# Kernel tuning notes

Measured on AMD Instinct MI355X. Metric: run time of the kernel, lower is better.

Reference implementation:

```python
import jax, jax.numpy as jnp
import numpy as np

HIDDEN = 1024
HEADS = 16
HEAD_DIM = HIDDEN // HEADS
B, S = 2, 2048


def setup_inputs() -> dict:
    key = jax.random.key(0)
    ks = jax.random.split(key, 11)
    std = 1.0 / np.sqrt(HIDDEN)
    return {
        "query": jax.random.normal(ks[0], (B, S, HIDDEN), dtype=jnp.float32),
        "key": jax.random.normal(ks[1], (B, S, HIDDEN), dtype=jnp.float32),
        "value": jax.random.normal(ks[2], (B, S, HIDDEN), dtype=jnp.float32),
        "Wq": jax.random.uniform(ks[3], (HIDDEN, HIDDEN), jnp.float32, -std, std),
        "bq": jax.random.uniform(ks[4], (HIDDEN,), jnp.float32, -std, std),
        "Wk": jax.random.uniform(ks[5], (HIDDEN, HIDDEN), jnp.float32, -std, std),
        "bk": jax.random.uniform(ks[6], (HIDDEN,), jnp.float32, -std, std),
        "Wv": jax.random.uniform(ks[7], (HIDDEN, HIDDEN), jnp.float32, -std, std),
        "bv": jax.random.uniform(ks[8], (HIDDEN,), jnp.float32, -std, std),
        "Wo": jax.random.uniform(ks[9], (HIDDEN, HIDDEN), jnp.float32, -std, std),
        "bo": jax.random.uniform(ks[10], (HIDDEN,), jnp.float32, -std, std),
    }


def reference(query, key, value, Wq, bq, Wk, bk, Wv, bv, Wo, bo):
    b = query.shape[0]
    scale = jnp.sqrt(jnp.float32(HEAD_DIM))
    # linear projections (torch Linear: x @ W.T + b), split into heads -> [b, h, s, d]
    def proj(x, W, bias):
        y = x @ W.T + bias
        return y.reshape(b, -1, HEADS, HEAD_DIM).transpose(0, 2, 1, 3)
    Q = proj(query, Wq, bq)
    K = proj(key, Wk, bk)
    V = proj(value, Wv, bv)
    scores = jnp.einsum("bhqd,bhkd->bhqk", Q, K) / scale
    attn = jax.nn.softmax(scores, axis=-1)
    ctx = jnp.einsum("bhqk,bhkd->bhqd", attn, V)
    ctx = ctx.transpose(0, 2, 1, 3).reshape(b, -1, HIDDEN)
    return ctx @ Wo.T + bo
```

## Files before the change

kernel.cpp:

```cpp
#include <hip/hip_runtime.h>

typedef __attribute__((ext_vector_type(8))) short short8;
typedef __attribute__((ext_vector_type(2))) float float2_t;
typedef __attribute__((ext_vector_type(4))) float float4_t;
typedef __attribute__((ext_vector_type(16))) float f32x16;
typedef __attribute__((ext_vector_type(4))) unsigned int uint4_t;
typedef __attribute__((ext_vector_type(2))) unsigned int uint2_t;
typedef unsigned short u16;

#define HIDDEN 1024
#define HDIM   64
#define SS     2048
#define TOK    4096
#define QSCALE 0.1803368801111137f

__device__ __forceinline__ unsigned int fbits(float f) {
  unsigned int x; __builtin_memcpy(&x, &f, 4); return x;
}
__device__ __forceinline__ u16 f2bf(float f) {
  return (u16)((fbits(f) + 0x8000u) >> 16);
}
__device__ __forceinline__ unsigned int pk2bf(float a, float b) {
  return __builtin_amdgcn_perm(fbits(b) + 0x8000u, fbits(a) + 0x8000u, 0x07060302);
}
__device__ __forceinline__ unsigned int pk2bf_t(float a, float b) {
  return __builtin_amdgcn_perm(fbits(b), fbits(a), 0x07060302);
}

__device__ __forceinline__ void gl_lds16(const u16* g, u16* l) {
  __builtin_amdgcn_global_load_lds(
      (const __attribute__((address_space(1))) unsigned int*)g,
      (__attribute__((address_space(3))) unsigned int*)l, 16, 0, 0);
}

__global__ __launch_bounds__(256) void convert_all(
    const float* __restrict__ w0, const float* __restrict__ w1,
    const float* __restrict__ w2, const float* __restrict__ w3,
    const float* __restrict__ x0, const float* __restrict__ x1,
    const float* __restrict__ x2, u16* __restrict__ Wall, u16* __restrict__ Xall) {
  int y = blockIdx.y;
  const float* src; u16* dst;
  if (y < 4) {
    if (blockIdx.x >= 512) return;
    src = y == 0 ? w0 : y == 1 ? w1 : y == 2 ? w2 : w3;
    dst = Wall + ((size_t)y << 20);
  } else {
    src = y == 4 ? x0 : y == 5 ? x1 : x2;
    dst = Xall + ((size_t)(y - 4) << 22);
  }
  int g = (blockIdx.x * 256 + threadIdx.x) * 8;
  float4_t a = *(const float4_t*)(src + g);
  float4_t b = *(const float4_t*)(src + g + 4);
  uint4_t o;
  o.x = pk2bf(a[0], a[1]); o.y = pk2bf(a[2], a[3]);
  o.z = pk2bf(b[0], b[1]); o.w = pk2bf(b[2], b[3]);
  *(uint4_t*)(dst + g) = o;
}

template<int MTILES, bool AXF32, bool OUTF32>
__device__ __forceinline__ void gemm_dbuf(
    const void* __restrict__ X, const u16* __restrict__ Wb,
    const float* __restrict__ bias, void* __restrict__ Y, int mode, float oscale,
    u16* sA, u16* sB, int row0, int col0) {
  const int tid  = threadIdx.x;
  const int wv   = tid >> 6, lane = tid & 63, quad = lane >> 4, ln = lane & 15;
  const int wm   = (wv >> 1) * (MTILES * 16), wn = (wv & 1) * 64;
  constexpr int ASZ = MTILES * 32 * 64;
  constexpr int BSZ = 128 * 64;

  float4_t acc[MTILES][4];
#pragma unroll
  for (int i = 0; i < MTILES; i++)
#pragma unroll
    for (int j = 0; j < 4; j++) acc[i][j] = (float4_t)0.0f;

  auto stageB = [&](int buf, int kt) {
    const int k0 = kt * 64;
#pragma unroll
    for (int i = 0; i < 4; i++) {
      int idx = i * 256 + tid, r = idx >> 3, c = idx & 7;
      int gc = c ^ (r & 7);
      gl_lds16(Wb + (size_t)(col0 + r) * HIDDEN + k0 + gc * 8, sB + buf * BSZ + idx * 8);
    }
  };
  auto stageA_bf16 = [&](int buf, int kt) {
    const int k0 = kt * 64;
#pragma unroll
    for (int i = 0; i < MTILES; i++) {
      int idx = i * 256 + tid, r = idx >> 3, c = idx & 7;
      int gc = c ^ (r & 7);
      gl_lds16((const u16*)X + (size_t)(row0 + r) * HIDDEN + k0 + gc * 8,
               sA + buf * ASZ + idx * 8);
    }
  };
  auto loadA_f32 = [&](int kt, float4_t (&ax)[MTILES][2]) {
    const int k0 = kt * 64;
#pragma unroll
    for (int i = 0; i < MTILES; i++) {
      int idx = i * 256 + tid, r = idx >> 3, c = idx & 7;
      const float* p = (const float*)X + (size_t)(row0 + r) * HIDDEN + k0 + c * 8;
      ax[i][0] = *(const float4_t*)p;
      ax[i][1] = *(const float4_t*)(p + 4);
    }
  };
  auto writeA_f32 = [&](int buf, float4_t (&ax)[MTILES][2]) {
#pragma unroll
    for (int i = 0; i < MTILES; i++) {
      int idx = i * 256 + tid, r = idx >> 3, c = idx & 7;
      int pos = c ^ (r & 7);
      union { unsigned int u[4]; short8 s; } x;
      x.u[0] = pk2bf(ax[i][0][0], ax[i][0][1]); x.u[1] = pk2bf(ax[i][0][2], ax[i][0][3]);
      x.u[2] = pk2bf(ax[i][1][0], ax[i][1][1]); x.u[3] = pk2bf(ax[i][1][2], ax[i][1][3]);
      *(short8*)(sA + buf * ASZ + r * 64 + pos * 8) = x.s;
    }
  };

  if (AXF32) {
    float4_t ax0[MTILES][2];
    loadA_f32(0, ax0);
    stageB(0, 0);
    writeA_f32(0, ax0);
  } else {
    stageB(0, 0);
    stageA_bf16(0, 0);
  }
  __syncthreads();

#pragma unroll 2
  for (int kt = 0; kt < 16; ++kt) {
    const int cur = kt & 1;
    float4_t axn[MTILES][2];
    if (AXF32) { if (kt < 15) loadA_f32(kt + 1, axn); }
    if (kt < 15) {
      stageB(cur ^ 1, kt + 1);
      if (!AXF32) stageA_bf16(cur ^ 1, kt + 1);
    }
    const u16* A_ = sA + cur * ASZ;
    const u16* B_ = sB + cur * BSZ;

    short8 af[MTILES][2], bfr[4][2];
#pragma unroll
    for (int mt = 0; mt < MTILES; mt++)
#pragma unroll
      for (int kk = 0; kk < 2; kk++) {
        int r = wm + mt * 16 + ln;
        int ch = kk * 4 + quad;
        af[mt][kk] = *(const short8*)(A_ + r * 64 + (ch ^ (r & 7)) * 8);
      }
#pragma unroll
    for (int nt = 0; nt < 4; nt++)
#pragma unroll
      for (int kk = 0; kk < 2; kk++) {
        int r = wn + nt * 16 + ln;
        int ch = kk * 4 + quad;
        bfr[nt][kk] = *(const short8*)(B_ + r * 64 + (ch ^ (r & 7)) * 8);
      }
#pragma unroll
    for (int kk = 0; kk < 2; kk++)
#pragma unroll
      for (int mt = 0; mt < MTILES; mt++)
#pragma unroll
        for (int nt = 0; nt < 4; nt++)
          acc[mt][nt] = __builtin_amdgcn_mfma_f32_16x16x32_bf16(af[mt][kk], bfr[nt][kk], acc[mt][nt], 0, 0, 0);

    if (AXF32) { if (kt < 15) writeA_f32(cur ^ 1, axn); }
    __syncthreads();
  }

  float bcol[4];
#pragma unroll
  for (int nt = 0; nt < 4; nt++) bcol[nt] = bias[col0 + wn + nt * 16 + ln];
#pragma unroll
  for (int mt = 0; mt < MTILES; mt++)
#pragma unroll
    for (int nt = 0; nt < 4; nt++) {
      int n = col0 + wn + nt * 16 + ln;
#pragma unroll
      for (int r = 0; r < 4; r++) {
        int m = row0 + wm + mt * 16 + quad * 4 + r;
        float v = (acc[mt][nt][r] + bcol[nt]) * oscale;
        if (mode == 0) {
          if (OUTF32) ((float*)Y)[(size_t)m * HIDDEN + n] = v;
          else        ((u16*)Y)[(size_t)m * HIDDEN + n] = f2bf(v);
        } else {
          ((u16*)Y)[((size_t)(m >> 11) * HIDDEN + n) * SS + (m & 2047)] = f2bf(v);
        }
      }
    }
}

__global__ __launch_bounds__(256) void qkv_gemm_bf16(
    const u16* __restrict__ Xall, const u16* __restrict__ Wall,
    const float* __restrict__ bq, const float* __restrict__ bk, const float* __restrict__ bv,
    u16* __restrict__ Qp, u16* __restrict__ Kp, u16* __restrict__ Vt) {
  __shared__ u16 sA[2 * 128 * 64];
  __shared__ u16 sB[2 * 128 * 64];
  int z = blockIdx.z;
  int fid = blockIdx.x, g = fid & 7, j = fid >> 3;
  int xb = j & 7, yb = g + 8 * (j >> 3);
  const u16* X = Xall + ((size_t)z << 22);
  const u16* W = Wall + ((size_t)z << 20);
  const float* Bp = z == 0 ? bq : z == 1 ? bk : bv;
  u16* Y = z == 0 ? Qp : z == 1 ? Kp : Vt;
  int mode = (z == 2) ? 1 : 0;
  float sc = (z == 0) ? QSCALE : 1.0f;
  gemm_dbuf<4, false, false>(X, W, Bp, Y, mode, sc, sA, sB, yb * 128, xb * 128);
}

__global__ __launch_bounds__(256) void qkv_gemm_f32(
    const float* __restrict__ xq, const float* __restrict__ xk, const float* __restrict__ xv,
    const u16* __restrict__ Wall,
    const float* __restrict__ bq, const float* __restrict__ bk, const float* __restrict__ bv,
    u16* __restrict__ Qp, u16* __restrict__ Kp, u16* __restrict__ Vt) {
  __shared__ u16 sA[2 * 128 * 64];
  __shared__ u16 sB[2 * 128 * 64];
  int z = blockIdx.z;
  int fid = blockIdx.x, g = fid & 7, j = fid >> 3;
  int xb = j & 7, yb = g + 8 * (j >> 3);
  const float* X = z == 0 ? xq : z == 1 ? xk : xv;
  const u16* W = Wall + ((size_t)z << 20);
  const float* Bp = z == 0 ? bq : z == 1 ? bk : bv;
  u16* Y = z == 0 ? Qp : z == 1 ? Kp : Vt;
  int mode = (z == 2) ? 1 : 0;
  float sc = (z == 0) ? QSCALE : 1.0f;
  gemm_dbuf<4, true, false>(X, W, Bp, Y, mode, sc, sA, sB, yb * 128, xb * 128);
}

__global__ __launch_bounds__(256) void out_gemm(
    const u16* __restrict__ X, const u16* __restrict__ Wob,
    const float* __restrict__ bias, float* __restrict__ Y) {
  __shared__ u16 sA[2 * 64 * 64];
  __shared__ u16 sB[2 * 128 * 64];
  int fid = blockIdx.x, g = fid & 7, j = fid >> 3;
  int xb = j & 7, yb = g + 8 * (j >> 3);
  gemm_dbuf<2, false, true>(X, Wob, bias, Y, 0, 1.0f, sA, sB, yb * 64, xb * 128);
}

__global__ __launch_bounds__(256, 2) void attn(
    const u16* __restrict__ Qp, const u16* __restrict__ Kp,
    const u16* __restrict__ Vt, u16* __restrict__ Ctx) {
  __shared__ u16 sK[2][128 * 64];
  __shared__ u16 sV[2][64 * 128];
  const int tid  = threadIdx.x;
  const int wv   = tid >> 6, lane = tid & 63;
  const int l5   = lane >> 5, ln = lane & 31;
  const int f = blockIdx.x;
  const int qt = f >> 5, g = f & 31, h = g >> 1, b = g & 1;
  const int row0w = qt * 128 + wv * 32;

  short8 qf[4];
#pragma unroll
  for (int kk = 0; kk < 4; ++kk)
    qf[kk] = *(const short8*)(Qp + (size_t)(b * SS + row0w + ln) * HIDDEN
                              + h * HDIM + kk * 16 + l5 * 8);

  f32x16 oacc[2];
  oacc[0] = (f32x16)0.0f; oacc[1] = (f32x16)0.0f;
  float dsum = 0.f;

  auto stage = [&](int buf, int kt) {
#pragma unroll
    for (int p = 0; p < 4; ++p) {
      int off = p * 256 + tid;
      { int r = off >> 3, c = off & 7;  int gc = c ^ (r & 7);
        gl_lds16(Kp + (size_t)(b * SS + kt * 128 + r) * HIDDEN + h * HDIM + gc * 8,
                 &sK[buf][0] + off * 8); }
      { int r = off >> 4, c = off & 15; int gc = c ^ (r & 15);
        gl_lds16(Vt + ((size_t)b * HIDDEN + h * HDIM + r) * SS + kt * 128 + gc * 8,
                 &sV[buf][0] + off * 8); }
    }
  };

  stage(0, 0);
  __syncthreads();

#pragma unroll 2
  for (int kt = 0; kt < 16; ++kt) {
    const int cur = kt & 1;
    if (kt < 15) stage(cur ^ 1, kt + 1);
    const u16* K_ = &sK[cur][0];
    const u16* V_ = &sV[cur][0];

    f32x16 st[4];
    __builtin_amdgcn_s_setprio(1);
#pragma unroll
    for (int kgg = 0; kgg < 4; ++kgg) {
      st[kgg] = (f32x16)0.0f;
#pragma unroll
      for (int kk = 0; kk < 4; ++kk) {
        int r = kgg * 32 + ln;
        int ch = kk * 2 + l5;
        short8 kf = *(const short8*)(K_ + r * 64 + ((ch ^ (r & 7))) * 8);
        st[kgg] = __builtin_amdgcn_mfma_f32_32x32x16_bf16(kf, qf[kk], st[kgg], 0, 0, 0);
      }
    }
    __builtin_amdgcn_s_setprio(0);

#pragma unroll
    for (int kgg = 0; kgg < 4; ++kgg) {
      union PF { unsigned int u[4]; short8 s; };
      PF pfr[2];
      {
        float p[16];
#pragma unroll
        for (int r = 0; r < 16; ++r)
          p[r] = __builtin_amdgcn_exp2f(fminf(st[kgg][r], 80.f));
        float2_t t0 = (float2_t){p[0], p[1]}   + (float2_t){p[2], p[3]};
        float2_t t1 = (float2_t){p[4], p[5]}   + (float2_t){p[6], p[7]};
        float2_t t2 = (float2_t){p[8], p[9]}   + (float2_t){p[10], p[11]};
        float2_t t3 = (float2_t){p[12], p[13]} + (float2_t){p[14], p[15]};
        float2_t t4 = (t0 + t1) + (t2 + t3);
        dsum += t4.x + t4.y;
        unsigned int pk[8];
#pragma unroll
        for (int i = 0; i < 8; ++i) pk[i] = pk2bf_t(p[2 * i], p[2 * i + 1]);
        uint2_t r02 = __builtin_amdgcn_permlane32_swap(pk[0], pk[2], false, false);
        uint2_t r13 = __builtin_amdgcn_permlane32_swap(pk[1], pk[3], false, false);
        uint2_t r46 = __builtin_amdgcn_permlane32_swap(pk[4], pk[6], false, false);
        uint2_t r57 = __builtin_amdgcn_permlane32_swap(pk[5], pk[7], false, false);
        pfr[0].u[0] = r02.x; pfr[0].u[1] = r13.x;
        pfr[0].u[2] = r02.y; pfr[0].u[3] = r13.y;
        pfr[1].u[0] = r46.x; pfr[1].u[1] = r57.x;
        pfr[1].u[2] = r46.y; pfr[1].u[3] = r57.y;
      }

      __builtin_amdgcn_s_setprio(1);
#pragma unroll
      for (int ks = 0; ks < 2; ++ks) {
        int ch = (kgg * 2 + ks) * 2 + l5;
#pragma unroll
        for (int dg = 0; dg < 2; ++dg) {
          int r = dg * 32 + ln;
          short8 vf = *(const short8*)(V_ + r * 128 + ((ch ^ (r & 15))) * 8);
          oacc[dg] = __builtin_amdgcn_mfma_f32_32x32x16_bf16(vf, pfr[ks].s, oacc[dg], 0, 0, 0);
        }
      }
      __builtin_amdgcn_s_setprio(0);
    }
    __syncthreads();
  }

  float s = dsum + __shfl_xor(dsum, 32, 64);
  float inv = 1.0f / s;

  u16* ep = ((u16*)sK) + wv * 2048;
  {
    int row = ln;
#pragma unroll
    for (int dg = 0; dg < 2; ++dg)
#pragma unroll
      for (int i = 0; i < 4; ++i) {
        uint2_t w;
        w.x = pk2bf(oacc[dg][4 * i] * inv,     oacc[dg][4 * i + 1] * inv);
        w.y = pk2bf(oacc[dg][4 * i + 2] * inv, oacc[dg][4 * i + 3] * inv);
        int c = dg * 4 + i;
        *(uint2_t*)(ep + row * 64 + ((c ^ (row & 7))) * 8 + l5 * 4) = w;
      }
  }
#pragma unroll
  for (int ps = 0; ps < 4; ++ps) {
    int r = ps * 8 + (lane >> 3);
    int c = lane & 7;
    short8 o8 = *(const short8*)(ep + r * 64 + ((c ^ (r & 7))) * 8);
    *(short8*)(Ctx + (size_t)(b * SS + row0w + r) * HIDDEN + h * HDIM + c * 8) = o8;
  }
}

extern "C" void kernel_launch(void* const* d_in, const int* in_sizes, int n_in,
                              void* d_out, int out_size, void* d_ws, size_t ws_size,
                              hipStream_t stream) {
  const float* q  = (const float*)d_in[0];
  const float* k  = (const float*)d_in[1];
  const float* v  = (const float*)d_in[2];
  const float* Wq = (const float*)d_in[3];
  const float* bq = (const float*)d_in[4];
  const float* Wk = (const float*)d_in[5];
  const float* bk = (const float*)d_in[6];
  const float* Wv = (const float*)d_in[7];
  const float* bv = (const float*)d_in[8];
  const float* Wo = (const float*)d_in[9];
  const float* bo = (const float*)d_in[10];

  u16* Qp   = (u16*)d_ws;
  u16* Kp   = Qp + (size_t)TOK * HIDDEN;
  u16* Vt   = Kp + (size_t)TOK * HIDDEN;
  u16* Wall = Vt + (size_t)TOK * HIDDEN;
  u16* Xall = Wall + (4u << 20);
  u16* Cx   = Qp;
  bool useX = ws_size >= (size_t)56 * 1024 * 1024;

  dim3 blk(256);
  if (useX) {
    hipLaunchKernelGGL(convert_all, dim3(2048, 7), blk, 0, stream,
                       Wq, Wk, Wv, Wo, q, k, v, Wall, Xall);
    hipLaunchKernelGGL(qkv_gemm_bf16, dim3(256, 1, 3), blk, 0, stream,
                       Xall, Wall, bq, bk, bv, Qp, Kp, Vt);
  } else {
    hipLaunchKernelGGL(convert_all, dim3(512, 4), blk, 0, stream,
                       Wq, Wk, Wv, Wo, q, k, v, Wall, Wall);
    hipLaunchKernelGGL(qkv_gemm_f32, dim3(256, 1, 3), blk, 0, stream,
                       q, k, v, Wall, bq, bk, bv, Qp, Kp, Vt);
  }
  hipLaunchKernelGGL(attn, dim3(512), blk, 0, stream, Qp, Kp, Vt, Cx);
  hipLaunchKernelGGL(out_gemm, dim3(512), blk, 0, stream,
                     Cx, Wall + (3u << 20), bo, (float*)d_out);
}
```

Before: 220.2 us.

## Pipeline bf16 GEMM loads two tiles ahead with explicit vmcnt waits

Splits the GEMM helper into a bf16-input path and an fp32-input path. The bf16 path (QKV bf16 GEMM and output GEMM) now issues direct-to-LDS loads two K-tiles ahead into the double buffer. It waits on them with partial s_waitcnt vmcnt counts and raw barriers instead of a full __syncthreads per iteration. This is meant to keep global loads in flight across the MFMA work, at the cost of a hand-counted vmcnt that must match the exact number of loads issued.

```diff
diff --git a/kernel.cpp b/kernel.cpp
--- a/kernel.cpp
+++ b/kernel.cpp
@@ -57,9 +57,9 @@
   *(uint4_t*)(dst + g) = o;
 }
 
-template<int MTILES, bool AXF32, bool OUTF32>
-__device__ __forceinline__ void gemm_dbuf(
-    const void* __restrict__ X, const u16* __restrict__ Wb,
+template<int MTILES, bool OUTF32>
+__device__ __forceinline__ void gemm_ctd(
+    const u16* __restrict__ X, const u16* __restrict__ Wb,
     const float* __restrict__ bias, void* __restrict__ Y, int mode, float oscale,
     u16* sA, u16* sB, int row0, int col0) {
   const int tid  = threadIdx.x;
@@ -67,6 +67,7 @@
   const int wm   = (wv >> 1) * (MTILES * 16), wn = (wv & 1) * 64;
   constexpr int ASZ = MTILES * 32 * 64;
   constexpr int BSZ = 128 * 64;
+  constexpr int NLOADS = MTILES + 4;
 
   float4_t acc[MTILES][4];
 #pragma unroll
@@ -74,7 +75,7 @@
 #pragma unroll
     for (int j = 0; j < 4; j++) acc[i][j] = (float4_t)0.0f;
 
-  auto stageB = [&](int buf, int kt) {
+  auto stage = [&](int buf, int kt) {
     const int k0 = kt * 64;
 #pragma unroll
     for (int i = 0; i < 4; i++) {
@@ -82,15 +83,105 @@
       int gc = c ^ (r & 7);
       gl_lds16(Wb + (size_t)(col0 + r) * HIDDEN + k0 + gc * 8, sB + buf * BSZ + idx * 8);
     }
-  };
-  auto stageA_bf16 = [&](int buf, int kt) {
-    const int k0 = kt * 64;
 #pragma unroll
     for (int i = 0; i < MTILES; i++) {
       int idx = i * 256 + tid, r = idx >> 3, c = idx & 7;
       int gc = c ^ (r & 7);
-      gl_lds16((const u16*)X + (size_t)(row0 + r) * HIDDEN + k0 + gc * 8,
-               sA + buf * ASZ + idx * 8);
+      gl_lds16(X + (size_t)(row0 + r) * HIDDEN + k0 + gc * 8, sA + buf * ASZ + idx * 8);
+    }
+  };
+
+  stage(0, 0);
+  stage(1, 1);
+  asm volatile("s_waitcnt vmcnt(%0)" :: "n"(NLOADS) : "memory");
+  __builtin_amdgcn_s_barrier();
+
+#pragma unroll 2
+  for (int kt = 0; kt < 16; ++kt) {
+    const int cur = kt & 1;
+    const u16* A_ = sA + cur * ASZ;
+    const u16* B_ = sB + cur * BSZ;
+
+    short8 af[MTILES][2], bfr[4][2];
+#pragma unroll
+    for (int mt = 0; mt < MTILES; mt++)
+#pragma unroll
+      for (int kk = 0; kk < 2; kk++) {
+        int r = wm + mt * 16 + ln;
+        int ch = kk * 4 + quad;
+        af[mt][kk] = *(const short8*)(A_ + r * 64 + (ch ^ (r & 7)) * 8);
+      }
+#pragma unroll
+    for (int nt = 0; nt < 4; nt++)
+#pragma unroll
+      for (int kk = 0; kk < 2; kk++) {
+        int r = wn + nt * 16 + ln;
+        int ch = kk * 4 + quad;
+        bfr[nt][kk] = *(const short8*)(B_ + r * 64 + (ch ^ (r & 7)) * 8);
+      }
+#pragma unroll
+    for (int kk = 0; kk < 2; kk++)
+#pragma unroll
+      for (int mt = 0; mt < MTILES; mt++)
+#pragma unroll
+        for (int nt = 0; nt < 4; nt++)
+          acc[mt][nt] = __builtin_amdgcn_mfma_f32_16x16x32_bf16(af[mt][kk], bfr[nt][kk], acc[mt][nt], 0, 0, 0);
+
+    __builtin_amdgcn_s_barrier();
+    if (kt < 14) stage(cur, kt + 2);
+    if (kt < 15) {
+      if (kt < 14) asm volatile("s_waitcnt vmcnt(%0)" :: "n"(NLOADS) : "memory");
+      else         asm volatile("s_waitcnt vmcnt(0)" ::: "memory");
+      __builtin_amdgcn_s_barrier();
+    }
+  }
+
+  float bcol[4];
+#pragma unroll
+  for (int nt = 0; nt < 4; nt++) bcol[nt] = bias[col0 + wn + nt * 16 + ln];
+#pragma unroll
+  for (int mt = 0; mt < MTILES; mt++)
+#pragma unroll
+    for (int nt = 0; nt < 4; nt++) {
+      int n = col0 + wn + nt * 16 + ln;
+#pragma unroll
+      for (int r = 0; r < 4; r++) {
+        int m = row0 + wm + mt * 16 + quad * 4 + r;
+        float v = (acc[mt][nt][r] + bcol[nt]) * oscale;
+        if (mode == 0) {
+          if (OUTF32) ((float*)Y)[(size_t)m * HIDDEN + n] = v;
+          else        ((u16*)Y)[(size_t)m * HIDDEN + n] = f2bf(v);
+        } else {
+          ((u16*)Y)[((size_t)(m >> 11) * HIDDEN + n) * SS + (m & 2047)] = f2bf(v);
+        }
+      }
+    }
+}
+
+template<int MTILES, bool OUTF32>
+__device__ __forceinline__ void gemm_dbuf_f32(
+    const float* __restrict__ X, const u16* __restrict__ Wb,
+    const float* __restrict__ bias, void* __restrict__ Y, int mode, float oscale,
+    u16* sA, u16* sB, int row0, int col0) {
+  const int tid  = threadIdx.x;
+  const int wv   = tid >> 6, lane = tid & 63, quad = lane >> 4, ln = lane & 15;
+  const int wm   = (wv >> 1) * (MTILES * 16), wn = (wv & 1) * 64;
+  constexpr int ASZ = MTILES * 32 * 64;
+  constexpr int BSZ = 128 * 64;
+
+  float4_t acc[MTILES][4];
+#pragma unroll
+  for (int i = 0; i < MTILES; i++)
+#pragma unroll
+    for (int j = 0; j < 4; j++) acc[i][j] = (float4_t)0.0f;
+
+  auto stageB = [&](int buf, int kt) {
+    const int k0 = kt * 64;
+#pragma unroll
+    for (int i = 0; i < 4; i++) {
+      int idx = i * 256 + tid, r = idx >> 3, c = idx & 7;
+      int gc = c ^ (r & 7);
+      gl_lds16(Wb + (size_t)(col0 + r) * HIDDEN + k0 + gc * 8, sB + buf * BSZ + idx * 8);
     }
   };
   auto loadA_f32 = [&](int kt, float4_t (&ax)[MTILES][2]) {
@@ -98,7 +189,7 @@
 #pragma unroll
     for (int i = 0; i < MTILES; i++) {
       int idx = i * 256 + tid, r = idx >> 3, c = idx & 7;
-      const float* p = (const float*)X + (size_t)(row0 + r) * HIDDEN + k0 + c * 8;
+      const float* p = X + (size_t)(row0 + r) * HIDDEN + k0 + c * 8;
       ax[i][0] = *(const float4_t*)p;
       ax[i][1] = *(const float4_t*)(p + 4);
     }
@@ -115,14 +206,11 @@
     }
   };
 
-  if (AXF32) {
+  {
     float4_t ax0[MTILES][2];
     loadA_f32(0, ax0);
     stageB(0, 0);
     writeA_f32(0, ax0);
-  } else {
-    stageB(0, 0);
-    stageA_bf16(0, 0);
   }
   __syncthreads();
 
@@ -130,11 +218,7 @@
   for (int kt = 0; kt < 16; ++kt) {
     const int cur = kt & 1;
     float4_t axn[MTILES][2];
-    if (AXF32) { if (kt < 15) loadA_f32(kt + 1, axn); }
-    if (kt < 15) {
-      stageB(cur ^ 1, kt + 1);
-      if (!AXF32) stageA_bf16(cur ^ 1, kt + 1);
-    }
+    if (kt < 15) { loadA_f32(kt + 1, axn); stageB(cur ^ 1, kt + 1); }
     const u16* A_ = sA + cur * ASZ;
     const u16* B_ = sB + cur * BSZ;
 
@@ -163,7 +247,7 @@
         for (int nt = 0; nt < 4; nt++)
           acc[mt][nt] = __builtin_amdgcn_mfma_f32_16x16x32_bf16(af[mt][kk], bfr[nt][kk], acc[mt][nt], 0, 0, 0);
 
-    if (AXF32) { if (kt < 15) writeA_f32(cur ^ 1, axn); }
+    if (kt < 15) writeA_f32(cur ^ 1, axn);
     __syncthreads();
   }
 
@@ -204,7 +288,7 @@
   u16* Y = z == 0 ? Qp : z == 1 ? Kp : Vt;
   int mode = (z == 2) ? 1 : 0;
   float sc = (z == 0) ? QSCALE : 1.0f;
-  gemm_dbuf<4, false, false>(X, W, Bp, Y, mode, sc, sA, sB, yb * 128, xb * 128);
+  gemm_ctd<4, false>(X, W, Bp, Y, mode, sc, sA, sB, yb * 128, xb * 128);
 }
 
 __global__ __launch_bounds__(256) void qkv_gemm_f32(
@@ -223,7 +307,7 @@
   u16* Y = z == 0 ? Qp : z == 1 ? Kp : Vt;
   int mode = (z == 2) ? 1 : 0;
   float sc = (z == 0) ? QSCALE : 1.0f;
-  gemm_dbuf<4, true, false>(X, W, Bp, Y, mode, sc, sA, sB, yb * 128, xb * 128);
+  gemm_dbuf_f32<4, false>(X, W, Bp, Y, mode, sc, sA, sB, yb * 128, xb * 128);
 }
 
 __global__ __launch_bounds__(256) void out_gemm(
@@ -233,7 +317,7 @@
   __shared__ u16 sB[2 * 128 * 64];
   int fid = blockIdx.x, g = fid & 7, j = fid >> 3;
   int xb = j & 7, yb = g + 8 * (j >> 3);
-  gemm_dbuf<2, false, true>(X, Wob, bias, Y, 0, 1.0f, sA, sB, yb * 64, xb * 128);
+  gemm_ctd<2, true>(X, Wob, bias, Y, 0, 1.0f, sA, sB, yb * 64, xb * 128);
 }
 
 __global__ __launch_bounds__(256, 2) void attn(
```

New measurement: 219.0 us. No clear change (-0.5%).
